# Kernel optimization log

Hardware: AMD Instinct MI355X
Metric: run time of the kernel (lower is better)

Reference implementation:

```python
import jax, jax.numpy as jnp
import numpy as np

N = 100000
E = 1600000
F_IN = 256
H1, C1 = 8, 8          # conv1: 8 heads x 8 channels -> 64
H2, C2 = 1, 32         # conv2: 1 head x num_classes
SLOPE = 0.2


def gat_conv(x, src, dst, n, W, a_src, a_dst, b, heads, out):
    # x: [n, f_in]; W: [f_in, heads*out]; a_src/a_dst: [heads, out]; b: [heads*out]
    h = (x @ W).reshape(n, heads, out)                       # [n, H, C]
    s = jnp.sum(h * a_src, axis=-1)                          # [n, H]
    d = jnp.sum(h * a_dst, axis=-1)                          # [n, H]
    e = jax.nn.leaky_relu(s[src] + d[dst], SLOPE)            # [e, H]
    m = jax.ops.segment_max(e, dst, num_segments=n)          # stable segment softmax
    ex = jnp.exp(e - m[dst])
    z = jax.ops.segment_sum(ex, dst, num_segments=n)
    alpha = ex / (z[dst] + 1e-16)                            # [e, H]
    msg = alpha[:, :, None] * h[src]                         # [e, H, C]
    agg = jax.ops.segment_sum(msg, dst, num_segments=n)      # [n, H, C]
    return agg.reshape(n, heads * out) + b


def setup_inputs() -> dict:
    key = jax.random.key(0)
    ks = jax.random.split(key, 10)
    x = jax.random.normal(ks[0], (N, F_IN), dtype=jnp.float32)
    edge_index = jax.random.randint(ks[1], (2, E), 0, N, dtype=jnp.int32)
    sc = 0.05
    W1 = jax.random.normal(ks[2], (F_IN, H1 * C1), dtype=jnp.float32) * sc
    att_src1 = jax.random.normal(ks[3], (H1, C1), dtype=jnp.float32) * sc
    att_dst1 = jax.random.normal(ks[4], (H1, C1), dtype=jnp.float32) * sc
    b1 = jnp.zeros((H1 * C1,), dtype=jnp.float32)
    W2 = jax.random.normal(ks[5], (H1 * C1, H2 * C2), dtype=jnp.float32) * sc
    att_src2 = jax.random.normal(ks[6], (H2, C2), dtype=jnp.float32) * sc
    att_dst2 = jax.random.normal(ks[7], (H2, C2), dtype=jnp.float32) * sc
    b2 = jnp.zeros((H2 * C2,), dtype=jnp.float32)
    return {"x": x, "edge_index": edge_index, "W1": W1, "att_src1": att_src1,
            "att_dst1": att_dst1, "b1": b1, "W2": W2, "att_src2": att_src2,
            "att_dst2": att_dst2, "b2": b2}


def reference(x, edge_index, W1, att_src1, att_dst1, b1, W2, att_src2, att_dst2, b2):
    # add self loops (PyG GATConv default)
    loops = jnp.arange(N, dtype=edge_index.dtype)
    src = jnp.concatenate([edge_index[0], loops])
    dst = jnp.concatenate([edge_index[1], loops])
    # dropout layers are identity in eval mode
    h = gat_conv(x, src, dst, N, W1, att_src1, att_dst1, b1, H1, C1)
    h = jax.nn.elu(h)
    h = gat_conv(h, src, dst, N, W2, att_src2, att_dst2, b2, H2, C2)
    return jax.nn.log_softmax(h, axis=1)
```

## Files before the change

kernel.cpp:

```cpp
#include <hip/hip_runtime.h>
#include <hip/hip_bf16.h>

#define N_NODES 100000
#define N_EDGES 1600000
#define N_TOT   (N_EDGES + N_NODES)
#define F_IN    256
#define F1      64
#define H1      8
#define C1      8
#define F2      32
#define SLOPE   0.2f

#define NB_G    ((N_NODES + 255) / 256)
#define NB_X    3125

#define EB      4096
#define NB1     ((N_EDGES + EB - 1) / EB)
#define BW      256
#define NBKT    ((N_NODES + BW - 1) / BW)

typedef unsigned int  uint;
typedef unsigned short ushort;
typedef __attribute__((ext_vector_type(8))) short bf16x8;
typedef __attribute__((ext_vector_type(4))) float f32x4;
typedef __attribute__((ext_vector_type(2))) float f32x2;

__device__ inline ushort f2bf(float f) {
    uint u = __float_as_uint(f);
    uint r = u + 0x7fffu + ((u >> 16) & 1u);
    return (ushort)(r >> 16);
}
__device__ inline float bflo(uint u) { return __uint_as_float(u << 16); }
__device__ inline float bfhi(uint u) { return __uint_as_float(u & 0xffff0000u); }
__device__ inline uint pk2bf(float a, float b) {
    __hip_bfloat162 h = __float22bfloat162_rn(make_float2(a, b));
    union { __hip_bfloat162 h; uint u; } cv; cv.h = h;
    return cv.u;
}

__device__ inline void bucket_bases(const int* __restrict__ colsum,
                                    int* sc, int* sb, int tid) {
    const int i0 = 2 * tid, i1 = 2 * tid + 1;
    const int a0 = (i0 < NBKT) ? colsum[i0] : 0;
    const int a1 = (i1 < NBKT) ? colsum[i1] : 0;
    sc[tid] = a0 + a1;
    __syncthreads();
    for (int off = 1; off < 256; off <<= 1) {
        int t = (tid >= off) ? sc[tid - off] : 0;
        __syncthreads();
        sc[tid] += t;
        __syncthreads();
    }
    const int excl = sc[tid] - (a0 + a1);
    if (i0 < NBKT)  sb[i0] = excl;
    if (i1 <= NBKT) sb[i1] = excl + a0;
    __syncthreads();
}

__global__ __launch_bounds__(256) void k_p1w(
        const int* __restrict__ ei, const float* __restrict__ W1,
        const float* __restrict__ x,
        int* __restrict__ bcnt, ushort* __restrict__ w1b,
        ushort* __restrict__ xb) {
    __shared__ int H[NBKT];
    const int tid = threadIdx.x;
    if (blockIdx.x < NB_X) {
        const size_t base = (size_t)blockIdx.x * 8192;
#pragma unroll
        for (int r = 0; r < 8; ++r) {
            const size_t idx = base + (size_t)r * 1024 + tid * 4;
            const float4 v = *(const float4*)(x + idx);
            *(uint2*)(xb + idx) = make_uint2(pk2bf(v.x, v.y), pk2bf(v.z, v.w));
        }
        return;
    }
    if (blockIdx.x == NB_X) {
        for (int i = 0; i < 64; ++i) {
            const int e = i * 256 + tid;
            const int k = e >> 6, n = e & 63;
            w1b[((k >> 3) * 64 + n) * 8 + (k & 7)] = f2bf(W1[e]);
        }
        return;
    }
    const int blk = blockIdx.x - NB_X - 1;
    for (int j = tid; j < NBKT; j += 256) H[j] = 0;
    __syncthreads();
    const int e0 = blk * EB;
    const int lim = (e0 + EB < N_EDGES) ? e0 + EB : N_EDGES;
    for (int i = e0 + tid; i < lim; i += 256)
        atomicAdd(&H[ei[N_EDGES + i] >> 8], 1);
    __syncthreads();
    for (int j = tid; j < NBKT; j += 256)
        bcnt[j * NB1 + blk] = H[j];
}

__global__ __launch_bounds__(64) void k_p2(
        int* __restrict__ bcnt, int* __restrict__ colsum) {
    const int col = blockIdx.x, lane = threadIdx.x;
    int carry = 0;
    for (int c0 = 0; c0 < NB1; c0 += 64) {
        const int idx = c0 + lane;
        const int v = (idx < NB1) ? bcnt[col * NB1 + idx] : 0;
        int s = v;
#pragma unroll
        for (int off = 1; off < 64; off <<= 1) {
            int u = __shfl_up(s, off);
            if (lane >= off) s += u;
        }
        if (idx < NB1) bcnt[col * NB1 + idx] = carry + s - v;
        carry += __shfl(s, 63);
    }
    if (lane == 0) colsum[col] = carry;
}

__global__ __launch_bounds__(256) void k_p3(
        const int* __restrict__ ei, const int* __restrict__ bcnt,
        const int* __restrict__ colsum, uint* __restrict__ tmp) {
    __shared__ int sc[256];
    __shared__ int cur[NBKT + 1];
    const int tid = threadIdx.x, blk = blockIdx.x;
    bucket_bases(colsum, sc, cur, tid);
    for (int b = tid; b < NBKT; b += 256) cur[b] += bcnt[b * NB1 + blk];
    __syncthreads();
    const int e0 = blk * EB;
    const int lim = (e0 + EB < N_EDGES) ? e0 + EB : N_EDGES;
    for (int i = e0 + tid; i < lim; i += 256) {
        const int s = ei[i], d = ei[N_EDGES + i];
        const int pos = atomicAdd(&cur[d >> 8], 1);
        tmp[pos] = ((uint)(d & 255) << 24) | (uint)s;
    }
}

__global__ __launch_bounds__(256) void k_final_gemm(
        const uint* __restrict__ tmp, const int* __restrict__ colsum,
        int* __restrict__ row_ptr, int* __restrict__ srcs,
        const ushort* __restrict__ xb, const ushort* __restrict__ w1b,
        const float* __restrict__ as1, const float* __restrict__ ad1,
        ushort* __restrict__ h1b, float* __restrict__ s1,
        float* __restrict__ d1) {
    __shared__ union {
        struct { int sc[256]; int sb[NBKT + 1]; int cur[BW]; } f;
        ushort B[F_IN * F1];
        ushort S[4][64][66];
    } sm;
    const int tid = threadIdx.x;

    if (blockIdx.x < NBKT) {
        const int b = blockIdx.x;
        bucket_bases(colsum, sm.f.sc, sm.f.sb, tid);
        sm.f.cur[tid] = 0;
        __syncthreads();
        const int lo = sm.f.sb[b], hi = sm.f.sb[b + 1];
        for (int i = lo + tid; i < hi; i += 256)
            atomicAdd(&sm.f.cur[tmp[i] >> 24], 1);
        __syncthreads();
        const int n = b * BW + tid;
        const int myc = sm.f.cur[tid];
        const int v = (n < N_NODES) ? myc + 1 : 0;
        __syncthreads();
        sm.f.sc[tid] = v;
        __syncthreads();
        for (int off = 1; off < 256; off <<= 1) {
            int t = (tid >= off) ? sm.f.sc[tid - off] : 0;
            __syncthreads();
            sm.f.sc[tid] += t;
            __syncthreads();
        }
        const int rp = lo + b * BW + (sm.f.sc[tid] - v);
        if (n < N_NODES) {
            row_ptr[n] = rp;
            srcs[rp] = n;
        }
        if (b == NBKT - 1 && tid == 255) row_ptr[N_NODES] = N_TOT;
        sm.f.cur[tid] = rp + 1;
        __syncthreads();
        for (int i = lo + tid; i < hi; i += 256) {
            const uint u = tmp[i];
            const int pos = atomicAdd(&sm.f.cur[u >> 24], 1);
            srcs[pos] = (int)(u & 0xFFFFFFu);
        }
        return;
    }

    {
        const uint4* s4 = (const uint4*)w1b;
        uint4* d4 = (uint4*)sm.B;
#pragma unroll
        for (int i = 0; i < 8; ++i)
            d4[i * 256 + tid] = s4[i * 256 + tid];
    }
    __syncthreads();

    const int wave = tid >> 6, lane = tid & 63;
    const int q = lane >> 4, ln = lane & 15;
    const int rowbase = (blockIdx.x - NBKT) * 256 + wave * 64;

    f32x4 acc[4][4];
#pragma unroll
    for (int mt = 0; mt < 4; ++mt)
#pragma unroll
        for (int nt = 0; nt < 4; ++nt) acc[mt][nt] = (f32x4){0.f, 0.f, 0.f, 0.f};

    const ushort* xrow[4];
#pragma unroll
    for (int mt = 0; mt < 4; ++mt) {
        const int r = rowbase + mt * 16 + ln;
        const int rc = r < N_NODES ? r : N_NODES - 1;
        xrow[mt] = xb + (size_t)rc * F_IN + q * 8;
    }

#pragma unroll 4
    for (int t = 0; t < 8; ++t) {
        bf16x8 bfr[4];
#pragma unroll
        for (int nt = 0; nt < 4; ++nt)
            bfr[nt] = *(const bf16x8*)&sm.B[((t * 4 + q) * 64 + nt * 16 + ln) * 8];
        bf16x8 af[4];
#pragma unroll
        for (int mt = 0; mt < 4; ++mt)
            af[mt] = *(const bf16x8*)(xrow[mt] + t * 32);
#pragma unroll
        for (int mt = 0; mt < 4; ++mt)
#pragma unroll
            for (int nt = 0; nt < 4; ++nt)
                acc[mt][nt] = __builtin_amdgcn_mfma_f32_16x16x32_bf16(
                                  af[mt], bfr[nt], acc[mt][nt], 0, 0, 0);
    }
    __syncthreads();

#pragma unroll
    for (int mt = 0; mt < 4; ++mt)
#pragma unroll
        for (int nt = 0; nt < 4; ++nt)
#pragma unroll
            for (int r = 0; r < 4; ++r)
                sm.S[wave][mt * 16 + q * 4 + r][nt * 16 + ln] = f2bf(acc[mt][nt][r]);
    __syncthreads();

    const int node = rowbase + lane;
    if (node >= N_NODES) return;
    const uint* srow = (const uint*)&sm.S[wave][lane][0];
    float sacc[H1], dacc[H1];
#pragma unroll
    for (int h = 0; h < H1; ++h) { sacc[h] = 0.f; dacc[h] = 0.f; }
    uint4* hout = (uint4*)(h1b + (size_t)node * F1);
#pragma unroll
    for (int p4 = 0; p4 < 8; ++p4) {
        const uint u0 = srow[p4 * 4 + 0], u1 = srow[p4 * 4 + 1];
        const uint u2 = srow[p4 * 4 + 2], u3 = srow[p4 * 4 + 3];
        hout[p4] = make_uint4(u0, u1, u2, u3);
        const float c[8] = {bflo(u0), bfhi(u0), bflo(u1), bfhi(u1),
                            bflo(u2), bfhi(u2), bflo(u3), bfhi(u3)};
#pragma unroll
        for (int j = 0; j < 8; ++j) {
            sacc[p4] += c[j] * as1[p4 * 8 + j];
            dacc[p4] += c[j] * ad1[p4 * 8 + j];
        }
    }
    float4* s4 = (float4*)(s1 + (size_t)node * H1);
    float4* d4 = (float4*)(d1 + (size_t)node * H1);
    s4[0] = make_float4(sacc[0], sacc[1], sacc[2], sacc[3]);
    s4[1] = make_float4(sacc[4], sacc[5], sacc[6], sacc[7]);
    d4[0] = make_float4(dacc[0], dacc[1], dacc[2], dacc[3]);
    d4[1] = make_float4(dacc[4], dacc[5], dacc[6], dacc[7]);
}

__global__ __launch_bounds__(256) void k_agg1(
        const int* __restrict__ row_ptr, const int* __restrict__ srcs,
        const ushort* __restrict__ h1b, const float* __restrict__ s1,
        const float* __restrict__ d1, const float* __restrict__ b1,
        const float* __restrict__ W2, const float* __restrict__ as2,
        const float* __restrict__ ad2,
        ushort* __restrict__ h2b, float* __restrict__ s2,
        float* __restrict__ d2) {
    __shared__ float sx[4][64];
    const int wid = (blockIdx.x * 256 + threadIdx.x) >> 6;
    if (wid >= N_NODES) return;
    const int w = threadIdx.x >> 6;
    const int lane = threadIdx.x & 63;
    const int q = lane >> 3;
    const int c = lane & 7;
    const float dh = d1[(size_t)wid * H1 + c];
    const int beg = row_ptr[wid], end = row_ptr[wid + 1];
    const uint4* hv = (const uint4*)h1b;
    f32x2 A0 = {0.f, 0.f}, A1 = {0.f, 0.f}, A2 = {0.f, 0.f}, A3 = {0.f, 0.f};
    float z = 0.f;
    int i = beg + q;
    for (; i + 8 < end; i += 16) {
        const int sA = srcs[i], sB = srcs[i + 8];
        float eA = s1[(size_t)sA * H1 + c] + dh;
        float eB = s1[(size_t)sB * H1 + c] + dh;
        eA = fmaxf(eA, SLOPE * eA);
        eB = fmaxf(eB, SLOPE * eB);
        const float xA = __expf(eA), xB = __expf(eB);
        const uint4 UA = hv[(size_t)sA * 8 + c];
        const uint4 UB = hv[(size_t)sB * 8 + c];
        z += xA + xB;
        const f32x2 xa = {xA, xA}, xb2 = {xB, xB};
        A0 += xa * (f32x2){bflo(UA.x), bfhi(UA.x)};
        A1 += xa * (f32x2){bflo(UA.y), bfhi(UA.y)};
        A2 += xa * (f32x2){bflo(UA.z), bfhi(UA.z)};
        A3 += xa * (f32x2){bflo(UA.w), bfhi(UA.w)};
        A0 += xb2 * (f32x2){bflo(UB.x), bfhi(UB.x)};
        A1 += xb2 * (f32x2){bflo(UB.y), bfhi(UB.y)};
        A2 += xb2 * (f32x2){bflo(UB.z), bfhi(UB.z)};
        A3 += xb2 * (f32x2){bflo(UB.w), bfhi(UB.w)};
    }
    for (; i < end; i += 8) {
        const int sA = srcs[i];
        float eA = s1[(size_t)sA * H1 + c] + dh;
        eA = fmaxf(eA, SLOPE * eA);
        const float xA = __expf(eA);
        const uint4 UA = hv[(size_t)sA * 8 + c];
        z += xA;
        const f32x2 xa = {xA, xA};
        A0 += xa * (f32x2){bflo(UA.x), bfhi(UA.x)};
        A1 += xa * (f32x2){bflo(UA.y), bfhi(UA.y)};
        A2 += xa * (f32x2){bflo(UA.z), bfhi(UA.z)};
        A3 += xa * (f32x2){bflo(UA.w), bfhi(UA.w)};
    }
    f32x2 r0, r1;
    {
        const bool hi = lane & 8;
        f32x2 snd0 = hi ? A0 : A2, snd1 = hi ? A1 : A3;
        const f32x2 kp0 = hi ? A2 : A0, kp1 = hi ? A3 : A1;
        snd0.x = __shfl_xor(snd0.x, 8); snd0.y = __shfl_xor(snd0.y, 8);
        snd1.x = __shfl_xor(snd1.x, 8); snd1.y = __shfl_xor(snd1.y, 8);
        r0 = kp0 + snd0; r1 = kp1 + snd1;
    }
    {
        const bool hi = lane & 16;
        f32x2 snd = hi ? r0 : r1;
        const f32x2 kp = hi ? r1 : r0;
        snd.x = __shfl_xor(snd.x, 16); snd.y = __shfl_xor(snd.y, 16);
        r0 = kp + snd;
    }
    float sv;
    {
        const bool hi = lane & 32;
        float snd = hi ? r0.x : r0.y;
        const float kp = hi ? r0.y : r0.x;
        snd = __shfl_xor(snd, 32);
        sv = kp + snd;
    }
    z += __shfl_xor(z, 8); z += __shfl_xor(z, 16); z += __shfl_xor(z, 32);

    const int j = (((lane >> 3) & 1) << 2) | (((lane >> 4) & 1) << 1)
                | ((lane >> 5) & 1);
    const int xi = c * 8 + j;
    const float zi = 1.f / (z + 1e-16f);
    float xv = sv * zi + b1[xi];
    xv = xv > 0.f ? xv : __expf(xv) - 1.f;
    sx[w][xi] = xv;
    __builtin_amdgcn_wave_barrier();

    const int kh = lane >> 5;
    const int oc = lane & 31;
    const float4* sxv = (const float4*)&sx[w][kh * 32];
    const float* wp0 = W2 + (size_t)(kh * 32) * F2 + oc;
    float acc = 0.f;
#pragma unroll
    for (int k4 = 0; k4 < 8; ++k4) {
        const float4 xv4 = sxv[k4];
        const float* wp = wp0 + (size_t)k4 * 4 * F2;
        acc += xv4.x * wp[0]      + xv4.y * wp[F2]
             + xv4.z * wp[2 * F2] + xv4.w * wp[3 * F2];
    }
    acc += __shfl_xor(acc, 32);

    float sA2 = acc * as2[oc], dA2 = acc * ad2[oc];
#pragma unroll
    for (int off = 1; off <= 16; off <<= 1) {
        sA2 += __shfl_xor(sA2, off);
        dA2 += __shfl_xor(dA2, off);
    }
    const float accp = __shfl_xor(acc, 1);
    if (lane < 32 && !(lane & 1))
        *(uint*)&h2b[(size_t)wid * F2 + oc] = pk2bf(acc, accp);
    if (lane == 0) { s2[wid] = sA2; d2[wid] = dA2; }
}

__global__ __launch_bounds__(256) void k_agg2(
        const int* __restrict__ row_ptr, const int* __restrict__ srcs,
        const ushort* __restrict__ h2b, const float* __restrict__ s2,
        const float* __restrict__ d2, const float* __restrict__ b2,
        float* __restrict__ out) {
    const int wid = (blockIdx.x * 256 + threadIdx.x) >> 6;
    if (wid >= N_NODES) return;
    const int lane = threadIdx.x & 63;
    const int q = lane >> 2;
    const int c = lane & 3;
    const float dn = d2[wid];
    const int beg = row_ptr[wid], end = row_ptr[wid + 1];
    const uint4* hv = (const uint4*)h2b;
    f32x2 A0 = {0.f, 0.f}, A1 = {0.f, 0.f}, A2 = {0.f, 0.f}, A3 = {0.f, 0.f};
    float z = 0.f;
    int i = beg + q;
    for (; i + 16 < end; i += 32) {
        const int sA = srcs[i], sB = srcs[i + 16];
        float eA = s2[sA] + dn;
        float eB = s2[sB] + dn;
        eA = fmaxf(eA, SLOPE * eA);
        eB = fmaxf(eB, SLOPE * eB);
        const float xA = __expf(eA), xB = __expf(eB);
        const uint4 UA = hv[(size_t)sA * 4 + c];
        const uint4 UB = hv[(size_t)sB * 4 + c];
        z += xA + xB;
        const f32x2 xa = {xA, xA}, xb2 = {xB, xB};
        A0 += xa * (f32x2){bflo(UA.x), bfhi(UA.x)};
        A1 += xa * (f32x2){bflo(UA.y), bfhi(UA.y)};
        A2 += xa * (f32x2){bflo(UA.z), bfhi(UA.z)};
        A3 += xa * (f32x2){bflo(UA.w), bfhi(UA.w)};
        A0 += xb2 * (f32x2){bflo(UB.x), bfhi(UB.x)};
        A1 += xb2 * (f32x2){bflo(UB.y), bfhi(UB.y)};
        A2 += xb2 * (f32x2){bflo(UB.z), bfhi(UB.z)};
        A3 += xb2 * (f32x2){bflo(UB.w), bfhi(UB.w)};
    }
    for (; i < end; i += 16) {
        const int sA = srcs[i];
        float eA = s2[sA] + dn;
        eA = fmaxf(eA, SLOPE * eA);
        const float xA = __expf(eA);
        const uint4 UA = hv[(size_t)sA * 4 + c];
        z += xA;
        const f32x2 xa = {xA, xA};
        A0 += xa * (f32x2){bflo(UA.x), bfhi(UA.x)};
        A1 += xa * (f32x2){bflo(UA.y), bfhi(UA.y)};
        A2 += xa * (f32x2){bflo(UA.z), bfhi(UA.z)};
        A3 += xa * (f32x2){bflo(UA.w), bfhi(UA.w)};
    }
    f32x2 r0, r1;
    {
        const bool hi = lane & 4;
        f32x2 snd0 = hi ? A0 : A2, snd1 = hi ? A1 : A3;
        const f32x2 kp0 = hi ? A2 : A0, kp1 = hi ? A3 : A1;
        snd0.x = __shfl_xor(snd0.x, 4); snd0.y = __shfl_xor(snd0.y, 4);
        snd1.x = __shfl_xor(snd1.x, 4); snd1.y = __shfl_xor(snd1.y, 4);
        r0 = kp0 + snd0; r1 = kp1 + snd1;
    }
    {
        const bool hi = lane & 8;
        f32x2 snd = hi ? r0 : r1;
        const f32x2 kp = hi ? r1 : r0;
        snd.x = __shfl_xor(snd.x, 8); snd.y = __shfl_xor(snd.y, 8);
        r0 = kp + snd;
    }
    float sv;
    {
        const bool hi = lane & 16;
        float snd = hi ? r0.x : r0.y;
        const float kp = hi ? r0.y : r0.x;
        snd = __shfl_xor(snd, 16);
        sv = kp + snd;
    }
    sv += __shfl_xor(sv, 32);
    z += __shfl_xor(z, 4); z += __shfl_xor(z, 8);
    z += __shfl_xor(z, 16); z += __shfl_xor(z, 32);

    const int j = (((lane >> 2) & 1) << 2) | (((lane >> 3) & 1) << 1)
                | ((lane >> 4) & 1);
    const int elem = c * 8 + j;
    const float zi = 1.f / (z + 1e-16f);
    const float v = sv * zi + b2[elem];
    float m = v;
#pragma unroll
    for (int off = 1; off <= 16; off <<= 1) m = fmaxf(m, __shfl_xor(m, off));
    float ssum = __expf(v - m);
#pragma unroll
    for (int off = 1; off <= 16; off <<= 1) ssum += __shfl_xor(ssum, off);
    const float lse = m + __logf(ssum);
    if (lane < 32) out[(size_t)wid * F2 + elem] = v - lse;
}

extern "C" void kernel_launch(void* const* d_in, const int* in_sizes, int n_in,
                              void* d_out, int out_size, void* d_ws, size_t ws_size,
                              hipStream_t stream) {
    const float* x   = (const float*)d_in[0];
    const int*   ei  = (const int*)d_in[1];
    const float* W1  = (const float*)d_in[2];
    const float* as1 = (const float*)d_in[3];
    const float* ad1 = (const float*)d_in[4];
    const float* b1  = (const float*)d_in[5];
    const float* W2  = (const float*)d_in[6];
    const float* as2 = (const float*)d_in[7];
    const float* ad2 = (const float*)d_in[8];
    const float* b2  = (const float*)d_in[9];
    float* out = (float*)d_out;

    ushort* xb  = (ushort*)d_ws;
    ushort* h1b = xb + (size_t)N_NODES * F_IN;
    ushort* h2b = h1b + (size_t)N_NODES * F1;
    ushort* w1b = h2b + (size_t)N_NODES * F2;
    float*  s1  = (float*)(w1b + F_IN * F1);
    float*  d1  = s1 + (size_t)N_NODES * H1;
    float*  s2  = d1 + (size_t)N_NODES * H1;
    float*  d2  = s2 + N_NODES;
    uint*   tmp = (uint*)(d2 + N_NODES);
    int* row_ptr = (int*)(tmp + N_EDGES);
    int* colsum  = row_ptr + N_NODES + 1;
    int* bcnt    = colsum + NBKT;
    int* srcs    = bcnt + (size_t)NBKT * NB1;

    const int nb_w = (N_NODES * 64 + 255) / 256;

    k_p1w<<<NB_X + 1 + NB1, 256, 0, stream>>>(ei, W1, x, bcnt, w1b, xb);
    k_p2<<<NBKT, 64, 0, stream>>>(bcnt, colsum);
    k_p3<<<NB1, 256, 0, stream>>>(ei, bcnt, colsum, tmp);
    k_final_gemm<<<NBKT + NB_G, 256, 0, stream>>>(tmp, colsum, row_ptr, srcs,
                                                  xb, w1b, as1, ad1,
                                                  h1b, s1, d1);
    k_agg1<<<nb_w, 256, 0, stream>>>(row_ptr, srcs, h1b, s1, d1, b1,
                                     W2, as2, ad2, h2b, s2, d2);
    k_agg2<<<nb_w, 256, 0, stream>>>(row_ptr, srcs, h2b, s2, d2, b2, out);
}
```

Baseline: 347.6 us.

## Vectorize edge bucket loads, use 32-bit offsets, and remap agg2 lanes per edge

Histogram and scatter passes now read two edge indices per thread via int2 loads. agg1 computes gather addresses with 32-bit byte offsets instead of size_t indexing, cutting 64-bit address arithmetic. agg2 now assigns 2 lanes per edge, each loading 32 bytes, so 32 edges are in flight per wave, with an extra shuffle stage in the reduction. This changes register pressure and load width in the aggregation kernel.

```diff
diff --git a/kernel.cpp b/kernel.cpp
--- a/kernel.cpp
+++ b/kernel.cpp
@@ -87,8 +87,11 @@
     __syncthreads();
     const int e0 = blk * EB;
     const int lim = (e0 + EB < N_EDGES) ? e0 + EB : N_EDGES;
-    for (int i = e0 + tid; i < lim; i += 256)
-        atomicAdd(&H[ei[N_EDGES + i] >> 8], 1);
+    for (int i = e0 + tid * 2; i < lim; i += 512) {
+        const int2 dd = *(const int2*)&ei[N_EDGES + i];
+        atomicAdd(&H[dd.x >> 8], 1);
+        atomicAdd(&H[dd.y >> 8], 1);
+    }
     __syncthreads();
     for (int j = tid; j < NBKT; j += 256)
         bcnt[j * NB1 + blk] = H[j];
@@ -124,10 +127,13 @@
     __syncthreads();
     const int e0 = blk * EB;
     const int lim = (e0 + EB < N_EDGES) ? e0 + EB : N_EDGES;
-    for (int i = e0 + tid; i < lim; i += 256) {
-        const int s = ei[i], d = ei[N_EDGES + i];
-        const int pos = atomicAdd(&cur[d >> 8], 1);
-        tmp[pos] = ((uint)(d & 255) << 24) | (uint)s;
+    for (int i = e0 + tid * 2; i < lim; i += 512) {
+        const int2 ss = *(const int2*)&ei[i];
+        const int2 dd = *(const int2*)&ei[N_EDGES + i];
+        const int p0 = atomicAdd(&cur[dd.x >> 8], 1);
+        tmp[p0] = ((uint)(dd.x & 255) << 24) | (uint)ss.x;
+        const int p1 = atomicAdd(&cur[dd.y >> 8], 1);
+        tmp[p1] = ((uint)(dd.y & 255) << 24) | (uint)ss.y;
     }
 }
 
@@ -282,19 +288,22 @@
     const int c = lane & 7;
     const float dh = d1[(size_t)wid * H1 + c];
     const int beg = row_ptr[wid], end = row_ptr[wid + 1];
-    const uint4* hv = (const uint4*)h1b;
+    const char* hP = (const char*)h1b;
+    const char* sP = (const char*)s1;
+    const uint hc16 = 16u * (uint)c;
+    const uint sc4 = 4u * (uint)c;
     f32x2 A0 = {0.f, 0.f}, A1 = {0.f, 0.f}, A2 = {0.f, 0.f}, A3 = {0.f, 0.f};
     float z = 0.f;
     int i = beg + q;
     for (; i + 8 < end; i += 16) {
-        const int sA = srcs[i], sB = srcs[i + 8];
-        float eA = s1[(size_t)sA * H1 + c] + dh;
-        float eB = s1[(size_t)sB * H1 + c] + dh;
+        const int nA = srcs[i], nB = srcs[i + 8];
+        float eA = *(const float*)(sP + ((uint)nA * 32u + sc4)) + dh;
+        float eB = *(const float*)(sP + ((uint)nB * 32u + sc4)) + dh;
         eA = fmaxf(eA, SLOPE * eA);
         eB = fmaxf(eB, SLOPE * eB);
         const float xA = __expf(eA), xB = __expf(eB);
-        const uint4 UA = hv[(size_t)sA * 8 + c];
-        const uint4 UB = hv[(size_t)sB * 8 + c];
+        const uint4 UA = *(const uint4*)(hP + ((uint)nA * 128u + hc16));
+        const uint4 UB = *(const uint4*)(hP + ((uint)nB * 128u + hc16));
         z += xA + xB;
         const f32x2 xa = {xA, xA}, xb2 = {xB, xB};
         A0 += xa * (f32x2){bflo(UA.x), bfhi(UA.x)};
@@ -307,11 +316,11 @@
         A3 += xb2 * (f32x2){bflo(UB.w), bfhi(UB.w)};
     }
     for (; i < end; i += 8) {
-        const int sA = srcs[i];
-        float eA = s1[(size_t)sA * H1 + c] + dh;
+        const int nA = srcs[i];
+        float eA = *(const float*)(sP + ((uint)nA * 32u + sc4)) + dh;
         eA = fmaxf(eA, SLOPE * eA);
         const float xA = __expf(eA);
-        const uint4 UA = hv[(size_t)sA * 8 + c];
+        const uint4 UA = *(const uint4*)(hP + ((uint)nA * 128u + hc16));
         z += xA;
         const f32x2 xa = {xA, xA};
         A0 += xa * (f32x2){bflo(UA.x), bfhi(UA.x)};
@@ -388,78 +397,77 @@
     const int wid = (blockIdx.x * 256 + threadIdx.x) >> 6;
     if (wid >= N_NODES) return;
     const int lane = threadIdx.x & 63;
-    const int q = lane >> 2;
-    const int c = lane & 3;
+    const int q = lane >> 1;
+    const int ch = lane & 1;
     const float dn = d2[wid];
     const int beg = row_ptr[wid], end = row_ptr[wid + 1];
-    const uint4* hv = (const uint4*)h2b;
+    const char* hP = (const char*)h2b;
+    const char* sP = (const char*)s2;
+    const uint ch32 = 32u * (uint)ch;
     f32x2 A0 = {0.f, 0.f}, A1 = {0.f, 0.f}, A2 = {0.f, 0.f}, A3 = {0.f, 0.f};
+    f32x2 A4 = {0.f, 0.f}, A5 = {0.f, 0.f}, A6 = {0.f, 0.f}, A7 = {0.f, 0.f};
     float z = 0.f;
-    int i = beg + q;
-    for (; i + 16 < end; i += 32) {
-        const int sA = srcs[i], sB = srcs[i + 16];
-        float eA = s2[sA] + dn;
-        float eB = s2[sB] + dn;
-        eA = fmaxf(eA, SLOPE * eA);
-        eB = fmaxf(eB, SLOPE * eB);
-        const float xA = __expf(eA), xB = __expf(eB);
-        const uint4 UA = hv[(size_t)sA * 4 + c];
-        const uint4 UB = hv[(size_t)sB * 4 + c];
-        z += xA + xB;
-        const f32x2 xa = {xA, xA}, xb2 = {xB, xB};
-        A0 += xa * (f32x2){bflo(UA.x), bfhi(UA.x)};
-        A1 += xa * (f32x2){bflo(UA.y), bfhi(UA.y)};
-        A2 += xa * (f32x2){bflo(UA.z), bfhi(UA.z)};
-        A3 += xa * (f32x2){bflo(UA.w), bfhi(UA.w)};
-        A0 += xb2 * (f32x2){bflo(UB.x), bfhi(UB.x)};
-        A1 += xb2 * (f32x2){bflo(UB.y), bfhi(UB.y)};
-        A2 += xb2 * (f32x2){bflo(UB.z), bfhi(UB.z)};
-        A3 += xb2 * (f32x2){bflo(UB.w), bfhi(UB.w)};
-    }
-    for (; i < end; i += 16) {
-        const int sA = srcs[i];
-        float eA = s2[sA] + dn;
+    for (int i = beg + q; i < end; i += 32) {
+        const int nA = srcs[i];
+        float eA = *(const float*)(sP + (uint)nA * 4u) + dn;
         eA = fmaxf(eA, SLOPE * eA);
         const float xA = __expf(eA);
-        const uint4 UA = hv[(size_t)sA * 4 + c];
+        const uint off = (uint)nA * 64u + ch32;
+        const uint4 U0 = *(const uint4*)(hP + off);
+        const uint4 U1 = *(const uint4*)(hP + off + 16);
         z += xA;
         const f32x2 xa = {xA, xA};
-        A0 += xa * (f32x2){bflo(UA.x), bfhi(UA.x)};
-        A1 += xa * (f32x2){bflo(UA.y), bfhi(UA.y)};
-        A2 += xa * (f32x2){bflo(UA.z), bfhi(UA.z)};
-        A3 += xa * (f32x2){bflo(UA.w), bfhi(UA.w)};
-    }
-    f32x2 r0, r1;
+        A0 += xa * (f32x2){bflo(U0.x), bfhi(U0.x)};
+        A1 += xa * (f32x2){bflo(U0.y), bfhi(U0.y)};
+        A2 += xa * (f32x2){bflo(U0.z), bfhi(U0.z)};
+        A3 += xa * (f32x2){bflo(U0.w), bfhi(U0.w)};
+        A4 += xa * (f32x2){bflo(U1.x), bfhi(U1.x)};
+        A5 += xa * (f32x2){bflo(U1.y), bfhi(U1.y)};
+        A6 += xa * (f32x2){bflo(U1.z), bfhi(U1.z)};
+        A7 += xa * (f32x2){bflo(U1.w), bfhi(U1.w)};
+    }
+    f32x2 r0, r1, r2, r3;
+    {
+        const bool hi = lane & 2;
+        f32x2 s0 = hi ? A0 : A4, s1v = hi ? A1 : A5;
+        f32x2 s2v = hi ? A2 : A6, s3v = hi ? A3 : A7;
+        const f32x2 k0 = hi ? A4 : A0, k1 = hi ? A5 : A1;
+        const f32x2 k2 = hi ? A6 : A2, k3 = hi ? A7 : A3;
+        s0.x = __shfl_xor(s0.x, 2); s0.y = __shfl_xor(s0.y, 2);
+        s1v.x = __shfl_xor(s1v.x, 2); s1v.y = __shfl_xor(s1v.y, 2);
+        s2v.x = __shfl_xor(s2v.x, 2); s2v.y = __shfl_xor(s2v.y, 2);
+        s3v.x = __shfl_xor(s3v.x, 2); s3v.y = __shfl_xor(s3v.y, 2);
+        r0 = k0 + s0; r1 = k1 + s1v; r2 = k2 + s2v; r3 = k3 + s3v;
+    }
     {
         const bool hi = lane & 4;
-        f32x2 snd0 = hi ? A0 : A2, snd1 = hi ? A1 : A3;
-        const f32x2 kp0 = hi ? A2 : A0, kp1 = hi ? A3 : A1;
-        snd0.x = __shfl_xor(snd0.x, 4); snd0.y = __shfl_xor(snd0.y, 4);
-        snd1.x = __shfl_xor(snd1.x, 4); snd1.y = __shfl_xor(snd1.y, 4);
-        r0 = kp0 + snd0; r1 = kp1 + snd1;
+        f32x2 s0 = hi ? r0 : r2, s1v = hi ? r1 : r3;
+        const f32x2 k0 = hi ? r2 : r0, k1 = hi ? r3 : r1;
+        s0.x = __shfl_xor(s0.x, 4); s0.y = __shfl_xor(s0.y, 4);
+        s1v.x = __shfl_xor(s1v.x, 4); s1v.y = __shfl_xor(s1v.y, 4);
+        r0 = k0 + s0; r1 = k1 + s1v;
     }
     {
         const bool hi = lane & 8;
-        f32x2 snd = hi ? r0 : r1;
-        const f32x2 kp = hi ? r1 : r0;
-        snd.x = __shfl_xor(snd.x, 8); snd.y = __shfl_xor(snd.y, 8);
-        r0 = kp + snd;
+        f32x2 s0 = hi ? r0 : r1;
+        const f32x2 k0 = hi ? r1 : r0;
+        s0.x = __shfl_xor(s0.x, 8); s0.y = __shfl_xor(s0.y, 8);
+        r0 = k0 + s0;
     }
     float sv;
     {
         const bool hi = lane & 16;
-        float snd = hi ? r0.x : r0.y;
-        const float kp = hi ? r0.y : r0.x;
-        snd = __shfl_xor(snd, 16);
-        sv = kp + snd;
+        float s0 = hi ? r0.x : r0.y;
+        const float k0 = hi ? r0.y : r0.x;
+        s0 = __shfl_xor(s0, 16);
+        sv = k0 + s0;
     }
     sv += __shfl_xor(sv, 32);
-    z += __shfl_xor(z, 4); z += __shfl_xor(z, 8);
+    z += __shfl_xor(z, 2); z += __shfl_xor(z, 4); z += __shfl_xor(z, 8);
     z += __shfl_xor(z, 16); z += __shfl_xor(z, 32);
 
-    const int j = (((lane >> 2) & 1) << 2) | (((lane >> 3) & 1) << 1)
-                | ((lane >> 4) & 1);
-    const int elem = c * 8 + j;
+    const int elem = ch * 16 + (((lane >> 1) & 1) << 3) | (((lane >> 2) & 1) << 2)
+                   | (((lane >> 3) & 1) << 1) | ((lane >> 4) & 1);
     const float zi = 1.f / (z + 1e-16f);
     const float v = sv * zi + b2[elem];
     float m = v;
```

Measured after the change: 345.0 us. About the same (-0.8%).
